# Kernel optimization log

Measured on AMD Instinct MI355X. Metric: run time of the kernel, lower is better.

The kernel has to match this reference:

```python
import jax, jax.numpy as jnp
import numpy as np

N_NODES = 100_000
N_EDGES = 3_200_000
D_IN, D_EDGE, D_HID, D_OUT = 8, 4, 32, 16
NEG_SLOPE = 0.2  # PyG GATv2Conv default


def setup_inputs() -> dict:
    key = jax.random.key(0)
    ks = jax.random.split(key, 13)
    s = 0.1
    return {
        "x": jax.random.normal(ks[0], (N_NODES, D_IN), jnp.float32),
        "edge_index": jax.random.randint(ks[1], (2, N_EDGES), 0, N_NODES, dtype=jnp.int64),
        "edge_attr": jax.random.normal(ks[2], (N_EDGES, D_EDGE), jnp.float32),
        "Wl1": jax.random.normal(ks[3], (D_IN, D_HID), jnp.float32) * s,
        "Wr1": jax.random.normal(ks[4], (D_IN, D_HID), jnp.float32) * s,
        "We1": jax.random.normal(ks[5], (D_EDGE, D_HID), jnp.float32) * s,
        "att1": jax.random.normal(ks[6], (D_HID,), jnp.float32) * s,
        "b1": jnp.zeros((D_HID,), jnp.float32),
        "Wl2": jax.random.normal(ks[7], (D_HID, D_OUT), jnp.float32) * s,
        "Wr2": jax.random.normal(ks[8], (D_HID, D_OUT), jnp.float32) * s,
        "We2": jax.random.normal(ks[9], (D_EDGE, D_OUT), jnp.float32) * s,
        "att2": jax.random.normal(ks[10], (D_OUT,), jnp.float32) * s,
        "b2": jnp.zeros((D_OUT,), jnp.float32),
    }


def _segment_softmax(score, seg, n):
    m = jax.ops.segment_max(score, seg, num_segments=n)
    e = jnp.exp(score - m[seg])
    z = jax.ops.segment_sum(e, seg, num_segments=n)
    return e / z[seg]


def _gatv2(x, src, dst, ea_raw, Wl, Wr, We, att, bias, n):
    # GATv2 (heads=1): score_ij = att . leaky_relu(Wl x_j + Wr x_i + We e_ij)
    xl = x @ Wl            # [N, d]
    xr = x @ Wr            # [N, d]
    ea = ea_raw @ We       # [E, d]
    h = jax.nn.leaky_relu(xl[src] + xr[dst] + ea, NEG_SLOPE)  # [E, d]
    score = h @ att        # [E]
    alpha = _segment_softmax(score, dst, n)
    out = jax.ops.segment_sum(alpha[:, None] * xl[src], dst, num_segments=n)
    return out + bias


def reference(x, edge_index, edge_attr, Wl1, Wr1, We1, att1, b1, Wl2, Wr2, We2, att2, b2):
    n = x.shape[0]
    src, dst = edge_index[0], edge_index[1]
    # add_self_loops=True with fill_value='mean': self-loop edge_attr = mean of
    # incoming raw edge_attr per target node (0 for isolated targets)
    ones = jnp.ones((src.shape[0],), x.dtype)
    cnt = jax.ops.segment_sum(ones, dst, num_segments=n)
    loop_attr = jax.ops.segment_sum(edge_attr, dst, num_segments=n) / jnp.maximum(cnt, 1.0)[:, None]
    ar = jnp.arange(n, dtype=src.dtype)
    src2 = jnp.concatenate([src, ar])
    dst2 = jnp.concatenate([dst, ar])
    ea2 = jnp.concatenate([edge_attr, loop_attr], axis=0)
    h = jax.nn.relu(_gatv2(x, src2, dst2, ea2, Wl1, Wr1, We1, att1, b1, n))
    out = _gatv2(h, src2, dst2, ea2, Wl2, Wr2, We2, att2, b2, n)
    return out.reshape(-1)
```

## Files before the change

kernel.cpp:

```cpp
#include <hip/hip_runtime.h>

#define NEG_SLOPE 0.2f
#define CHUNK 16384
#define KMAX  1600
#define CAP   3264
#define NBLKMAX 256

__global__ __launch_bounds__(1024) void k_bin(const int* __restrict__ ei,
                                              const float* __restrict__ eattr,
                                              int* __restrict__ cloff,
                                              int* __restrict__ ssrc,
                                              float4* __restrict__ seat,
                                              int E, int K) {
    __shared__ int s_off[KMAX + 1];
    __shared__ unsigned s_eid[CHUNK];
    int t = threadIdx.x;
    for (int i = t; i <= K; i += 1024) s_off[i] = 0;
    __syncthreads();
    int base = blockIdx.x * CHUNK;
    int end = min(base + CHUNK, E);
    int Ec = end - base;
    unsigned pack[CHUNK / 1024];
#pragma unroll
    for (int i = 0; i < CHUNK / 1024; i++) {
        int el = t + 1024 * i;
        pack[i] = 0xFFFFFFFFu;
        if (el < Ec) {
            int dst = ei[E + base + el];
            int b = dst >> 6;
            int r = atomicAdd(&s_off[b], 1);
            pack[i] = ((unsigned)b << 20) | ((unsigned)(dst & 63) << 14) | (unsigned)r;
        }
    }
    __syncthreads();
    if (t < 64) {
        int run = 0;
        for (int bb = 0; bb < K; bb += 64) {
            int b = bb + t;
            int v = (b < K) ? s_off[b] : 0;
            int x = v;
#pragma unroll
            for (int off = 1; off < 64; off <<= 1) {
                int y = __shfl_up(x, off, 64);
                if (t >= off) x += y;
            }
            if (b < K) s_off[b] = run + x - v;
            run += __shfl(x, 63, 64);
        }
        if (t == 0) s_off[K] = run;
    }
    __syncthreads();
#pragma unroll
    for (int i = 0; i < CHUNK / 1024; i++) {
        int el = t + 1024 * i;
        if (el < Ec) {
            unsigned p = pack[i];
            int b = p >> 20;
            int r = p & 0x3FFF;
            int dl = (p >> 14) & 63;
            s_eid[s_off[b] + r] = ((unsigned)dl << 14) | (unsigned)el;
        }
    }
    __syncthreads();
    for (int pos = t; pos < Ec; pos += 1024) {
        unsigned v = s_eid[pos];
        int el = v & 0x3FFF;
        int dl = v >> 14;
        int e = base + el;
        int src = ei[e];
        float4 a = *(const float4*)(eattr + 4ll * e);
        ssrc[base + pos] = src | (dl << 17);
        seat[base + pos] = a;
    }
    for (int i = t; i <= K; i += 1024)
        cloff[(long long)blockIdx.x * (K + 1) + i] = s_off[i];
}

__global__ void k_transp(const int* __restrict__ in, int* __restrict__ out, int R, int C) {
    __shared__ int tile[32][33];
    int c0 = blockIdx.x * 32, r0 = blockIdx.y * 32;
    int c = c0 + threadIdx.x, r = r0 + threadIdx.y;
    if (r < R && c < C) tile[threadIdx.y][threadIdx.x] = in[(long long)r * C + c];
    __syncthreads();
    int oc = r0 + threadIdx.x, orr = c0 + threadIdx.y;
    if (orr < C && oc < R) out[(long long)orr * R + oc] = tile[threadIdx.x][threadIdx.y];
}

__global__ void k_btot(const int* __restrict__ cloffT, int* __restrict__ bucketTotal,
                       int K, int NBLK) {
    int b = (blockIdx.x * blockDim.x + threadIdx.x) >> 6;
    int lane = threadIdx.x & 63;
    if (b >= K) return;
    const int* r0 = cloffT + (long long)b * NBLK;
    const int* r1 = r0 + NBLK;
    int s = 0;
    for (int c = lane; c < NBLK; c += 64) s += r1[c] - r0[c];
#pragma unroll
    for (int off = 32; off >= 1; off >>= 1) s += __shfl_xor(s, off, 64);
    if (lane == 0) bucketTotal[b] = s;
}

__global__ void k_scanK(const int* __restrict__ bucketTotal, int* __restrict__ slotBase,
                        int* __restrict__ qofs, int N, int K) {
    __shared__ int s[512];
    int t = threadIdx.x;
    int v[4];
    int sum = 0;
    int base = t * 4;
    for (int j = 0; j < 4; j++) {
        int b = base + j, x = 0;
        if (b < K) { int nb = min(64, N - (b << 6)); x = bucketTotal[b] + nb; }
        v[j] = sum;
        sum += x;
    }
    s[t] = sum;
    __syncthreads();
    for (int off = 1; off < 512; off <<= 1) {
        int x = (t >= off) ? s[t - off] : 0;
        __syncthreads();
        s[t] += x;
        __syncthreads();
    }
    int tb = s[t] - sum;
    for (int j = 0; j < 4; j++) {
        int b = base + j;
        if (b < K) slotBase[b] = tb + v[j];
    }
    if (t == 511) { slotBase[K] = s[511]; qofs[4ll * N] = s[511]; }
}

__global__ __launch_bounds__(512, 8) void k_perm(const int* __restrict__ ssrc,
                                                 const float4* __restrict__ seat,
                                                 const int* __restrict__ cloffT,
                                                 const int* __restrict__ slotBase,
                                                 int* __restrict__ qofs,
                                                 int* __restrict__ fsrc,
                                                 float4* __restrict__ feat,
                                                 int N, int K, int NBLK, int QDIV) {
    __shared__ int s_pack[CAP];
    __shared__ int s_g[CAP];
    __shared__ int co[NBLKMAX], qq[NBLKMAX + 1], sc[NBLKMAX];
    __shared__ int hist2[256], cur2[256], lst2[256], sc2[256];
    __shared__ int hist[64];
    __shared__ float lsum[64][4];
    int b = blockIdx.x, t = threadIdx.x;
    int nb = min(64, N - (b << 6));
    if (t < 256) { hist2[t] = 0; cur2[t] = 0; }
    if (t < 64) {
        lsum[t][0] = 0.f; lsum[t][1] = 0.f; lsum[t][2] = 0.f; lsum[t][3] = 0.f;
    }
    const int* r0 = cloffT + (long long)b * NBLK;
    const int* r1 = r0 + NBLK;
    int len = 0;
    if (t < NBLKMAX) {
        if (t < NBLK) { int c0v = r0[t]; len = r1[t] - c0v; co[t] = c0v; }
        sc[t] = (t < NBLK) ? len : 0;
    }
    __syncthreads();
    for (int off = 1; off < NBLKMAX; off <<= 1) {
        int x = 0;
        if (t < NBLKMAX && t >= off) x = sc[t - off];
        __syncthreads();
        if (t < NBLKMAX) sc[t] += x;
        __syncthreads();
    }
    if (t < NBLK) qq[t] = sc[t] - len;
    if (t == NBLKMAX - 1) qq[NBLK] = sc[NBLKMAX - 1];
    __syncthreads();
    int Eb = qq[NBLK];
    for (int i = t; i < Eb; i += 512) {
        int lo2 = 0, hi2 = NBLK;
        while (lo2 + 1 < hi2) { int mid = (lo2 + hi2) >> 1; if (qq[mid] <= i) lo2 = mid; else hi2 = mid; }
        int g = lo2 * CHUNK + co[lo2] + (i - qq[lo2]);
        int p = ssrc[g];
        int srcv = p & 0x1FFFF;
        int q = (unsigned)srcv / (unsigned)QDIV;
        s_pack[i] = p | (q << 23);
        s_g[i] = g;
        atomicAdd(&hist2[(((p >> 17) & 63) << 2) | q], 1);
    }
    __syncthreads();
    if (t < 64) {
        int c = hist2[4 * t] + hist2[4 * t + 1] + hist2[4 * t + 2] + hist2[4 * t + 3];
        hist[t] = c;
        if (t < nb) {
            int node = (b << 6) + t;
            int qs = (unsigned)node / (unsigned)QDIV;
            hist2[t * 4 + qs] += 1;
            cur2[t * 4 + qs] = 1;
        }
    }
    __syncthreads();
    if (t < 256) sc2[t] = hist2[t];
    __syncthreads();
    for (int off = 1; off < 256; off <<= 1) {
        int x = 0;
        if (t < 256 && t >= off) x = sc2[t - off];
        __syncthreads();
        if (t < 256) sc2[t] += x;
        __syncthreads();
    }
    if (t < 256) lst2[t] = sc2[t] - hist2[t];
    __syncthreads();
    int lo = slotBase[b];
    if (t < 256) {
        int dl = t >> 2;
        if (dl < nb)
            qofs[(((long long)((b << 6) + dl)) << 2) + (t & 3)] = lo + lst2[t];
    }
    for (int i = t; i < Eb; i += 512) {
        int p = s_pack[i];
        int dl = (p >> 17) & 63;
        int q = (p >> 23) & 3;
        int srcv = p & 0x1FFFF;
        int bin = (dl << 2) | q;
        int r = atomicAdd(&cur2[bin], 1);
        float4 a = seat[s_g[i]];
        long long pos = lo + lst2[bin] + r;
        fsrc[pos] = srcv;
        feat[pos] = a;
        atomicAdd(&lsum[dl][0], a.x);
        atomicAdd(&lsum[dl][1], a.y);
        atomicAdd(&lsum[dl][2], a.z);
        atomicAdd(&lsum[dl][3], a.w);
    }
    __syncthreads();
    if (t < nb) {
        int node = (b << 6) + t;
        int qs = (unsigned)node / (unsigned)QDIV;
        float inv = 1.f / fmaxf((float)hist[t], 1.f);
        long long pos = lo + lst2[t * 4 + qs];
        fsrc[pos] = node;
        feat[pos] = make_float4(lsum[t][0] * inv, lsum[t][1] * inv,
                                lsum[t][2] * inv, lsum[t][3] * inv);
    }
}

template <int DIN, int D>
__global__ void k_xform(const float* __restrict__ x, const float* __restrict__ Wl,
                        const float* __restrict__ Wr, float* __restrict__ xl,
                        float* __restrict__ xr, int N) {
    __shared__ float sWl[DIN * D], sWr[DIN * D];
    for (int i = threadIdx.x; i < DIN * D; i += blockDim.x) { sWl[i] = Wl[i]; sWr[i] = Wr[i]; }
    __syncthreads();
    int t = blockIdx.x * blockDim.x + threadIdx.x;
    if (t >= N * D) return;
    int n = t / D, d = t % D;
    const float* xp = x + (long long)n * DIN;
    float sl = 0.f, sr = 0.f;
#pragma unroll
    for (int k = 0; k < DIN; k++) {
        float xv = xp[k];
        sl += xv * sWl[k * D + d];
        sr += xv * sWr[k * D + d];
    }
    xl[t] = sl;
    xr[t] = sr;
}

template <int L>
__device__ __forceinline__ void gat_edge(bool valid, const float4& a, const float4& xlv,
                                         const float4& we0, const float4& we1,
                                         const float4& we2, const float4& we3,
                                         const float4& av, const float4& xrv,
                                         float4& acc, float& z) {
    float4 v;
    v.x = fmaf(a.x, we0.x, xrv.x); v.x = fmaf(a.y, we1.x, v.x);
    v.x = fmaf(a.z, we2.x, v.x);   v.x = fmaf(a.w, we3.x, v.x); v.x += xlv.x;
    v.y = fmaf(a.x, we0.y, xrv.y); v.y = fmaf(a.y, we1.y, v.y);
    v.y = fmaf(a.z, we2.y, v.y);   v.y = fmaf(a.w, we3.y, v.y); v.y += xlv.y;
    v.z = fmaf(a.x, we0.z, xrv.z); v.z = fmaf(a.y, we1.z, v.z);
    v.z = fmaf(a.z, we2.z, v.z);   v.z = fmaf(a.w, we3.z, v.z); v.z += xlv.z;
    v.w = fmaf(a.x, we0.w, xrv.w); v.w = fmaf(a.y, we1.w, v.w);
    v.w = fmaf(a.z, we2.w, v.w);   v.w = fmaf(a.w, we3.w, v.w); v.w += xlv.w;
    v.x = v.x > 0.f ? v.x : NEG_SLOPE * v.x;
    v.y = v.y > 0.f ? v.y : NEG_SLOPE * v.y;
    v.z = v.z > 0.f ? v.z : NEG_SLOPE * v.z;
    v.w = v.w > 0.f ? v.w : NEG_SLOPE * v.w;
    float sc = av.x * v.x + av.y * v.y + av.z * v.z + av.w * v.w;
#pragma unroll
    for (int off = L / 2; off >= 1; off >>= 1) sc += __shfl_xor(sc, off, 64);
    float ev = valid ? __expf(sc) : 0.f;
    z += ev;
    acc.x = fmaf(ev, xlv.x, acc.x);
    acc.y = fmaf(ev, xlv.y, acc.y);
    acc.z = fmaf(ev, xlv.z, acc.z);
    acc.w = fmaf(ev, xlv.w, acc.w);
}

template <int D, bool RELU>
__global__ void k_gat(const int* __restrict__ fsrc,
                      const float4* __restrict__ feat,
                      const int* __restrict__ qofs,
                      const float* __restrict__ xl, const float* __restrict__ xr,
                      const float* __restrict__ We, const float* __restrict__ att,
                      const float* __restrict__ bias, float* __restrict__ out, int N) {
    constexpr int L = D / 4;
    constexpr int G = 64 / L;
    int w = (blockIdx.x * blockDim.x + threadIdx.x) >> 6;
    int lane = threadIdx.x & 63;
    if (w >= N) return;
    int g = lane / L;
    int j = lane % L;
    int s0 = qofs[4 * w], s1 = qofs[4 * w + 4];
    int cnt = s1 - s0;

    const float4 we0 = *(const float4*)(We + 0 * D + 4 * j);
    const float4 we1 = *(const float4*)(We + 1 * D + 4 * j);
    const float4 we2 = *(const float4*)(We + 2 * D + 4 * j);
    const float4 we3 = *(const float4*)(We + 3 * D + 4 * j);
    const float4 av  = *(const float4*)(att + 4 * j);
    const float4 xrv = *(const float4*)(xr + (long long)w * D + 4 * j);

    float4 acc = make_float4(0.f, 0.f, 0.f, 0.f);
    float z = 0.f;

    int it = 0;
    for (; (it + 2) * G <= cnt; it += 2) {
        int sl = s0 + it * G + g;
        int srcA = fsrc[sl];
        int srcB = fsrc[sl + G];
        float4 aA = feat[sl];
        float4 aB = feat[sl + G];
        float4 xA = *(const float4*)(xl + (long long)srcA * D + 4 * j);
        float4 xB = *(const float4*)(xl + (long long)srcB * D + 4 * j);
        gat_edge<L>(true, aA, xA, we0, we1, we2, we3, av, xrv, acc, z);
        gat_edge<L>(true, aB, xB, we0, we1, we2, we3, av, xrv, acc, z);
    }
    for (; it * G < cnt; ++it) {
        int o = it * G + g;
        bool v = o < cnt;
        int sl = s0 + min(o, cnt - 1);
        int src = fsrc[sl];
        float4 a = feat[sl];
        float4 xv = *(const float4*)(xl + (long long)src * D + 4 * j);
        gat_edge<L>(v, a, xv, we0, we1, we2, we3, av, xrv, acc, z);
    }

#pragma unroll
    for (int off = 32; off >= L; off >>= 1) {
        acc.x += __shfl_xor(acc.x, off, 64);
        acc.y += __shfl_xor(acc.y, off, 64);
        acc.z += __shfl_xor(acc.z, off, 64);
        acc.w += __shfl_xor(acc.w, off, 64);
        z += __shfl_xor(z, off, 64);
    }

    if (g == 0) {
        float inv = 1.0f / z;
        float4 bv = *(const float4*)(bias + 4 * j);
        float4 o;
        o.x = acc.x * inv + bv.x;
        o.y = acc.y * inv + bv.y;
        o.z = acc.z * inv + bv.z;
        o.w = acc.w * inv + bv.w;
        if (RELU) {
            o.x = fmaxf(o.x, 0.f); o.y = fmaxf(o.y, 0.f);
            o.z = fmaxf(o.z, 0.f); o.w = fmaxf(o.w, 0.f);
        }
        *(float4*)(out + (long long)w * D + 4 * j) = o;
    }
}

extern "C" void kernel_launch(void* const* d_in, const int* in_sizes, int n_in,
                              void* d_out, int out_size, void* d_ws, size_t ws_size,
                              hipStream_t stream) {
    const float* x     = (const float*)d_in[0];
    const int*   ei    = (const int*)d_in[1];
    const float* eattr = (const float*)d_in[2];
    const float* Wl1   = (const float*)d_in[3];
    const float* Wr1   = (const float*)d_in[4];
    const float* We1   = (const float*)d_in[5];
    const float* att1  = (const float*)d_in[6];
    const float* b1    = (const float*)d_in[7];
    const float* Wl2   = (const float*)d_in[8];
    const float* Wr2   = (const float*)d_in[9];
    const float* We2   = (const float*)d_in[10];
    const float* att2  = (const float*)d_in[11];
    const float* b2    = (const float*)d_in[12];

    const int N = in_sizes[0] / 8;
    const int E = in_sizes[1] / 2;
    const int K = (N + 63) >> 6;
    const int NBLK = (E + CHUNK - 1) / CHUNK;
    const int QDIV = (N + 3) / 4;

    int* iws = (int*)d_ws;
    size_t o = 0;
    int* bucketTotal = iws + o; o += K;
    int* slotBase    = iws + o; o += K + 1;
    int* qofs        = iws + o; o += 4ll * N + 1;
    int* cloff       = iws + o; o += (size_t)NBLK * (K + 1);
    int* cloffT      = iws + o; o += (size_t)(K + 1) * NBLK;
    o = (o + 7) & ~(size_t)7;
    int*    fsrc = (int*)(iws + o);    o += (size_t)(E + N);
    o = (o + 3) & ~(size_t)3;
    float4* feat = (float4*)(iws + o); o += 4ll * (E + N);
    size_t stage = o;
    int*    ssrc = (int*)(iws + o);    o += (size_t)E;
    o = (o + 3) & ~(size_t)3;
    float4* seat = (float4*)(iws + o); o += 4ll * E;
    float* xl = (float*)(iws + stage);
    float* xr = xl + 32ll * N;
    float* h  = xr + 32ll * N;

    const int B = 256;
    auto cdiv = [](long long a, long long b) { return (int)((a + b - 1) / b); };

    k_bin<<<NBLK, 1024, 0, stream>>>(ei, eattr, cloff, ssrc, seat, E, K);
    dim3 tb(32, 32);
    k_transp<<<dim3(cdiv(K + 1, 32), cdiv(NBLK, 32)), tb, 0, stream>>>(cloff, cloffT, NBLK, K + 1);
    k_btot<<<cdiv(64ll * K, B), B, 0, stream>>>(cloffT, bucketTotal, K, NBLK);
    k_scanK<<<1, 512, 0, stream>>>(bucketTotal, slotBase, qofs, N, K);
    k_perm<<<K, 512, 0, stream>>>(ssrc, seat, cloffT, slotBase, qofs, fsrc, feat, N, K, NBLK, QDIV);

    k_xform<8, 32><<<cdiv(32ll * N, B), B, 0, stream>>>(x, Wl1, Wr1, xl, xr, N);
    k_gat<32, true><<<cdiv(N, 4), B, 0, stream>>>(fsrc, feat, qofs, xl, xr, We1, att1, b1, h, N);

    k_xform<32, 16><<<cdiv(16ll * N, B), B, 0, stream>>>(h, Wl2, Wr2, xl, xr, N);
    k_gat<16, false><<<cdiv(N, 4), B, 0, stream>>>(fsrc, feat, qofs, xl, xr, We2, att2, b2, (float*)d_out, N);
}
```

Measured before the change: 487.9 us.

## Halve bin chunk size, parallelize bucket scan, scatter directly without LDS staging

The binning kernel now works on 8192-edge chunks with 512 threads, which doubles the number of blocks. The single-wavefront serial scan over bucket counts becomes a block-wide Hillis-Steele scan with 4 buckets per thread. The shared edge-id staging array is removed, and each edge's src and attributes are written straight to their binned position. This cuts LDS use and the serial scan latency, but the direct scatter gives less coalesced global reads and writes, and the downstream transpose, total and perm stages must handle twice as many per-block offset rows.

```diff
diff --git a/kernel.cpp b/kernel.cpp
--- a/kernel.cpp
+++ b/kernel.cpp
@@ -1,29 +1,28 @@
 #include <hip/hip_runtime.h>
 
 #define NEG_SLOPE 0.2f
-#define CHUNK 16384
+#define CHUNK 8192
 #define KMAX  1600
 #define CAP   3264
-#define NBLKMAX 256
-
-__global__ __launch_bounds__(1024) void k_bin(const int* __restrict__ ei,
-                                              const float* __restrict__ eattr,
-                                              int* __restrict__ cloff,
-                                              int* __restrict__ ssrc,
-                                              float4* __restrict__ seat,
-                                              int E, int K) {
+#define NBLKMAX 512
+
+__global__ __launch_bounds__(512) void k_bin(const int* __restrict__ ei,
+                                             const float* __restrict__ eattr,
+                                             int* __restrict__ cloff,
+                                             int* __restrict__ ssrc,
+                                             float4* __restrict__ seat,
+                                             int E, int K) {
     __shared__ int s_off[KMAX + 1];
-    __shared__ unsigned s_eid[CHUNK];
+    __shared__ int s_scan[512];
     int t = threadIdx.x;
-    for (int i = t; i <= K; i += 1024) s_off[i] = 0;
+    for (int i = t; i <= K; i += 512) s_off[i] = 0;
     __syncthreads();
     int base = blockIdx.x * CHUNK;
-    int end = min(base + CHUNK, E);
-    int Ec = end - base;
-    unsigned pack[CHUNK / 1024];
-#pragma unroll
-    for (int i = 0; i < CHUNK / 1024; i++) {
-        int el = t + 1024 * i;
+    int Ec = min(CHUNK, E - base);
+    unsigned pack[CHUNK / 512];
+#pragma unroll
+    for (int i = 0; i < CHUNK / 512; i++) {
+        int el = t + 512 * i;
         pack[i] = 0xFFFFFFFFu;
         if (el < Ec) {
             int dst = ei[E + base + el];
@@ -33,46 +32,48 @@
         }
     }
     __syncthreads();
-    if (t < 64) {
-        int run = 0;
-        for (int bb = 0; bb < K; bb += 64) {
-            int b = bb + t;
-            int v = (b < K) ? s_off[b] : 0;
-            int x = v;
-#pragma unroll
-            for (int off = 1; off < 64; off <<= 1) {
-                int y = __shfl_up(x, off, 64);
-                if (t >= off) x += y;
-            }
-            if (b < K) s_off[b] = run + x - v;
-            run += __shfl(x, 63, 64);
-        }
-        if (t == 0) s_off[K] = run;
-    }
-    __syncthreads();
-#pragma unroll
-    for (int i = 0; i < CHUNK / 1024; i++) {
-        int el = t + 1024 * i;
+    int v4[4];
+    int sum = 0;
+    int b0 = t << 2;
+#pragma unroll
+    for (int jj = 0; jj < 4; jj++) {
+        int b = b0 + jj;
+        int x = (b <= K) ? s_off[b] : 0;
+        v4[jj] = sum;
+        sum += x;
+    }
+    s_scan[t] = sum;
+    __syncthreads();
+    for (int off = 1; off < 512; off <<= 1) {
+        int x = (t >= off) ? s_scan[t - off] : 0;
+        __syncthreads();
+        s_scan[t] += x;
+        __syncthreads();
+    }
+    int tb = s_scan[t] - sum;
+#pragma unroll
+    for (int jj = 0; jj < 4; jj++) {
+        int b = b0 + jj;
+        if (b <= K) s_off[b] = tb + v4[jj];
+    }
+    __syncthreads();
+#pragma unroll
+    for (int i = 0; i < CHUNK / 512; i++) {
+        int el = t + 512 * i;
         if (el < Ec) {
             unsigned p = pack[i];
             int b = p >> 20;
+            int dl = (p >> 14) & 63;
             int r = p & 0x3FFF;
-            int dl = (p >> 14) & 63;
-            s_eid[s_off[b] + r] = ((unsigned)dl << 14) | (unsigned)el;
+            int pos = s_off[b] + r;
+            int e = base + el;
+            int src = ei[e];
+            float4 a = *(const float4*)(eattr + 4ll * e);
+            ssrc[base + pos] = src | (dl << 17);
+            seat[base + pos] = a;
         }
     }
-    __syncthreads();
-    for (int pos = t; pos < Ec; pos += 1024) {
-        unsigned v = s_eid[pos];
-        int el = v & 0x3FFF;
-        int dl = v >> 14;
-        int e = base + el;
-        int src = ei[e];
-        float4 a = *(const float4*)(eattr + 4ll * e);
-        ssrc[base + pos] = src | (dl << 17);
-        seat[base + pos] = a;
-    }
-    for (int i = t; i <= K; i += 1024)
+    for (int i = t; i <= K; i += 512)
         cloff[(long long)blockIdx.x * (K + 1) + i] = s_off[i];
 }
 
@@ -407,7 +408,7 @@
     const int B = 256;
     auto cdiv = [](long long a, long long b) { return (int)((a + b - 1) / b); };
 
-    k_bin<<<NBLK, 1024, 0, stream>>>(ei, eattr, cloff, ssrc, seat, E, K);
+    k_bin<<<NBLK, 512, 0, stream>>>(ei, eattr, cloff, ssrc, seat, E, K);
     dim3 tb(32, 32);
     k_transp<<<dim3(cdiv(K + 1, 32), cdiv(NBLK, 32)), tb, 0, stream>>>(cloff, cloffT, NBLK, K + 1);
     k_btot<<<cdiv(64ll * K, B), B, 0, stream>>>(cloffT, bucketTotal, K, NBLK);
```

Result: slower. 502.9 us (+3.1%).

## Restructure CSR build with smaller chunks, 256-node buckets, and shared staging

Applied to the files above, without the earlier changes.

Changes the edge binning so each block handles 4096 edges and destinations are grouped into 256-node buckets instead of 64. k_bin now gathers src and edge_attr straight into shared memory at their sorted positions and then writes them out coalesced. k_perm runs 1024 threads per block, re-reads ssrc in a second pass instead of caching it in shared memory, and covers four times as many nodes per block. The aim is fewer, larger permutation blocks and coalesced staging writes, at the cost of doubled global reads in k_perm, a binary search over up to 1024 chunks per edge, and a larger cloff matrix.

```diff
diff --git a/kernel.cpp b/kernel.cpp
--- a/kernel.cpp
+++ b/kernel.cpp
@@ -1,10 +1,9 @@
 #include <hip/hip_runtime.h>
 
 #define NEG_SLOPE 0.2f
-#define CHUNK 16384
-#define KMAX  1600
-#define CAP   3264
-#define NBLKMAX 256
+#define CHUNK 4096
+#define KMAX  512
+#define NBLKMAX 1024
 
 __global__ __launch_bounds__(1024) void k_bin(const int* __restrict__ ei,
                                               const float* __restrict__ eattr,
@@ -13,13 +12,14 @@
                                               float4* __restrict__ seat,
                                               int E, int K) {
     __shared__ int s_off[KMAX + 1];
-    __shared__ unsigned s_eid[CHUNK];
+    __shared__ int s_scan[1024];
+    __shared__ int s_ssrc[CHUNK];
+    __shared__ float4 s_seat[CHUNK];
     int t = threadIdx.x;
     for (int i = t; i <= K; i += 1024) s_off[i] = 0;
     __syncthreads();
     int base = blockIdx.x * CHUNK;
-    int end = min(base + CHUNK, E);
-    int Ec = end - base;
+    int Ec = min(CHUNK, E - base);
     unsigned pack[CHUNK / 1024];
 #pragma unroll
     for (int i = 0; i < CHUNK / 1024; i++) {
@@ -27,28 +27,22 @@
         pack[i] = 0xFFFFFFFFu;
         if (el < Ec) {
             int dst = ei[E + base + el];
-            int b = dst >> 6;
+            int b = dst >> 8;
             int r = atomicAdd(&s_off[b], 1);
-            pack[i] = ((unsigned)b << 20) | ((unsigned)(dst & 63) << 14) | (unsigned)r;
+            pack[i] = ((unsigned)b << 20) | ((unsigned)(dst & 255) << 12) | (unsigned)r;
         }
     }
     __syncthreads();
-    if (t < 64) {
-        int run = 0;
-        for (int bb = 0; bb < K; bb += 64) {
-            int b = bb + t;
-            int v = (b < K) ? s_off[b] : 0;
-            int x = v;
-#pragma unroll
-            for (int off = 1; off < 64; off <<= 1) {
-                int y = __shfl_up(x, off, 64);
-                if (t >= off) x += y;
-            }
-            if (b < K) s_off[b] = run + x - v;
-            run += __shfl(x, 63, 64);
-        }
-        if (t == 0) s_off[K] = run;
-    }
+    int x0 = (t <= K) ? s_off[t] : 0;
+    s_scan[t] = x0;
+    __syncthreads();
+    for (int off = 1; off < 1024; off <<= 1) {
+        int y = (t >= off) ? s_scan[t - off] : 0;
+        __syncthreads();
+        s_scan[t] += y;
+        __syncthreads();
+    }
+    if (t <= K) s_off[t] = s_scan[t] - x0;
     __syncthreads();
 #pragma unroll
     for (int i = 0; i < CHUNK / 1024; i++) {
@@ -56,21 +50,18 @@
         if (el < Ec) {
             unsigned p = pack[i];
             int b = p >> 20;
-            int r = p & 0x3FFF;
-            int dl = (p >> 14) & 63;
-            s_eid[s_off[b] + r] = ((unsigned)dl << 14) | (unsigned)el;
+            int dl = (p >> 12) & 255;
+            int r = p & 0xFFF;
+            int pos = s_off[b] + r;
+            int e = base + el;
+            s_ssrc[pos] = ei[e] | (dl << 17);
+            s_seat[pos] = *(const float4*)(eattr + 4ll * e);
         }
     }
     __syncthreads();
     for (int pos = t; pos < Ec; pos += 1024) {
-        unsigned v = s_eid[pos];
-        int el = v & 0x3FFF;
-        int dl = v >> 14;
-        int e = base + el;
-        int src = ei[e];
-        float4 a = *(const float4*)(eattr + 4ll * e);
-        ssrc[base + pos] = src | (dl << 17);
-        seat[base + pos] = a;
+        ssrc[base + pos] = s_ssrc[pos];
+        seat[base + pos] = s_seat[pos];
     }
     for (int i = t; i <= K; i += 1024)
         cloff[(long long)blockIdx.x * (K + 1) + i] = s_off[i];
@@ -109,7 +100,7 @@
     int base = t * 4;
     for (int j = 0; j < 4; j++) {
         int b = base + j, x = 0;
-        if (b < K) { int nb = min(64, N - (b << 6)); x = bucketTotal[b] + nb; }
+        if (b < K) { int nb = min(256, N - (b << 8)); x = bucketTotal[b] + nb; }
         v[j] = sum;
         sum += x;
     }
@@ -129,93 +120,81 @@
     if (t == 511) { slotBase[K] = s[511]; qofs[4ll * N] = s[511]; }
 }
 
-__global__ __launch_bounds__(512, 8) void k_perm(const int* __restrict__ ssrc,
-                                                 const float4* __restrict__ seat,
-                                                 const int* __restrict__ cloffT,
-                                                 const int* __restrict__ slotBase,
-                                                 int* __restrict__ qofs,
-                                                 int* __restrict__ fsrc,
-                                                 float4* __restrict__ feat,
-                                                 int N, int K, int NBLK, int QDIV) {
-    __shared__ int s_pack[CAP];
-    __shared__ int s_g[CAP];
+__global__ __launch_bounds__(1024, 2) void k_perm(const int* __restrict__ ssrc,
+                                                  const float4* __restrict__ seat,
+                                                  const int* __restrict__ cloffT,
+                                                  const int* __restrict__ slotBase,
+                                                  int* __restrict__ qofs,
+                                                  int* __restrict__ fsrc,
+                                                  float4* __restrict__ feat,
+                                                  int N, int K, int NBLK, int QDIV) {
     __shared__ int co[NBLKMAX], qq[NBLKMAX + 1], sc[NBLKMAX];
-    __shared__ int hist2[256], cur2[256], lst2[256], sc2[256];
-    __shared__ int hist[64];
-    __shared__ float lsum[64][4];
+    __shared__ int hist2[1024], cur2[1024], lst2[1024], sc2[1024];
+    __shared__ int hist[256];
+    __shared__ float lsum[256][4];
     int b = blockIdx.x, t = threadIdx.x;
-    int nb = min(64, N - (b << 6));
-    if (t < 256) { hist2[t] = 0; cur2[t] = 0; }
-    if (t < 64) {
-        lsum[t][0] = 0.f; lsum[t][1] = 0.f; lsum[t][2] = 0.f; lsum[t][3] = 0.f;
-    }
+    int nb = min(256, N - (b << 8));
+    hist2[t] = 0; cur2[t] = 0;
+    if (t < 256) { lsum[t][0] = 0.f; lsum[t][1] = 0.f; lsum[t][2] = 0.f; lsum[t][3] = 0.f; }
     const int* r0 = cloffT + (long long)b * NBLK;
     const int* r1 = r0 + NBLK;
     int len = 0;
-    if (t < NBLKMAX) {
-        if (t < NBLK) { int c0v = r0[t]; len = r1[t] - c0v; co[t] = c0v; }
-        sc[t] = (t < NBLK) ? len : 0;
-    }
+    if (t < NBLK) { int c0v = r0[t]; len = r1[t] - c0v; co[t] = c0v; }
+    sc[t] = (t < NBLK) ? len : 0;
     __syncthreads();
     for (int off = 1; off < NBLKMAX; off <<= 1) {
-        int x = 0;
-        if (t < NBLKMAX && t >= off) x = sc[t - off];
-        __syncthreads();
-        if (t < NBLKMAX) sc[t] += x;
+        int x = (t >= off) ? sc[t - off] : 0;
+        __syncthreads();
+        sc[t] += x;
         __syncthreads();
     }
     if (t < NBLK) qq[t] = sc[t] - len;
     if (t == NBLKMAX - 1) qq[NBLK] = sc[NBLKMAX - 1];
     __syncthreads();
     int Eb = qq[NBLK];
-    for (int i = t; i < Eb; i += 512) {
+    for (int i = t; i < Eb; i += 1024) {
+        int lo2 = 0, hi2 = NBLK;
+        while (lo2 + 1 < hi2) { int mid = (lo2 + hi2) >> 1; if (qq[mid] <= i) lo2 = mid; else hi2 = mid; }
+        int g = lo2 * CHUNK + co[lo2] + (i - qq[lo2]);
+        int p = ssrc[g];
+        int q = (int)((unsigned)(p & 0x1FFFF) / (unsigned)QDIV);
+        atomicAdd(&hist2[(((p >> 17) & 255) << 2) | q], 1);
+    }
+    __syncthreads();
+    if (t < 256) {
+        int c = hist2[4 * t] + hist2[4 * t + 1] + hist2[4 * t + 2] + hist2[4 * t + 3];
+        hist[t] = c;
+        if (t < nb) {
+            int node = (b << 8) + t;
+            int qs = (int)((unsigned)node / (unsigned)QDIV);
+            hist2[4 * t + qs] += 1;
+            cur2[4 * t + qs] = 1;
+        }
+    }
+    __syncthreads();
+    sc2[t] = hist2[t];
+    __syncthreads();
+    for (int off = 1; off < 1024; off <<= 1) {
+        int x = (t >= off) ? sc2[t - off] : 0;
+        __syncthreads();
+        sc2[t] += x;
+        __syncthreads();
+    }
+    lst2[t] = sc2[t] - hist2[t];
+    __syncthreads();
+    int lo = slotBase[b];
+    if (t < 4 * nb) qofs[((long long)b << 10) + t] = lo + lst2[t];
+    for (int i = t; i < Eb; i += 1024) {
         int lo2 = 0, hi2 = NBLK;
         while (lo2 + 1 < hi2) { int mid = (lo2 + hi2) >> 1; if (qq[mid] <= i) lo2 = mid; else hi2 = mid; }
         int g = lo2 * CHUNK + co[lo2] + (i - qq[lo2]);
         int p = ssrc[g];
         int srcv = p & 0x1FFFF;
-        int q = (unsigned)srcv / (unsigned)QDIV;
-        s_pack[i] = p | (q << 23);
-        s_g[i] = g;
-        atomicAdd(&hist2[(((p >> 17) & 63) << 2) | q], 1);
-    }
-    __syncthreads();
-    if (t < 64) {
-        int c = hist2[4 * t] + hist2[4 * t + 1] + hist2[4 * t + 2] + hist2[4 * t + 3];
-        hist[t] = c;
-        if (t < nb) {
-            int node = (b << 6) + t;
-            int qs = (unsigned)node / (unsigned)QDIV;
-            hist2[t * 4 + qs] += 1;
-            cur2[t * 4 + qs] = 1;
-        }
-    }
-    __syncthreads();
-    if (t < 256) sc2[t] = hist2[t];
-    __syncthreads();
-    for (int off = 1; off < 256; off <<= 1) {
-        int x = 0;
-        if (t < 256 && t >= off) x = sc2[t - off];
-        __syncthreads();
-        if (t < 256) sc2[t] += x;
-        __syncthreads();
-    }
-    if (t < 256) lst2[t] = sc2[t] - hist2[t];
-    __syncthreads();
-    int lo = slotBase[b];
-    if (t < 256) {
-        int dl = t >> 2;
-        if (dl < nb)
-            qofs[(((long long)((b << 6) + dl)) << 2) + (t & 3)] = lo + lst2[t];
-    }
-    for (int i = t; i < Eb; i += 512) {
-        int p = s_pack[i];
-        int dl = (p >> 17) & 63;
-        int q = (p >> 23) & 3;
-        int srcv = p & 0x1FFFF;
+        int dl = (p >> 17) & 255;
+        int q = (int)((unsigned)srcv / (unsigned)QDIV);
         int bin = (dl << 2) | q;
         int r = atomicAdd(&cur2[bin], 1);
-        float4 a = seat[s_g[i]];
+        float4 a = seat[g];
         long long pos = lo + lst2[bin] + r;
         fsrc[pos] = srcv;
         feat[pos] = a;
@@ -226,10 +205,10 @@
     }
     __syncthreads();
     if (t < nb) {
-        int node = (b << 6) + t;
-        int qs = (unsigned)node / (unsigned)QDIV;
+        int node = (b << 8) + t;
+        int qs = (int)((unsigned)node / (unsigned)QDIV);
         float inv = 1.f / fmaxf((float)hist[t], 1.f);
-        long long pos = lo + lst2[t * 4 + qs];
+        long long pos = lo + lst2[4 * t + qs];
         fsrc[pos] = node;
         feat[pos] = make_float4(lsum[t][0] * inv, lsum[t][1] * inv,
                                 lsum[t][2] * inv, lsum[t][3] * inv);
@@ -381,7 +360,7 @@
 
     const int N = in_sizes[0] / 8;
     const int E = in_sizes[1] / 2;
-    const int K = (N + 63) >> 6;
+    const int K = (N + 255) >> 8;
     const int NBLK = (E + CHUNK - 1) / CHUNK;
     const int QDIV = (N + 3) / 4;
 
@@ -412,7 +391,7 @@
     k_transp<<<dim3(cdiv(K + 1, 32), cdiv(NBLK, 32)), tb, 0, stream>>>(cloff, cloffT, NBLK, K + 1);
     k_btot<<<cdiv(64ll * K, B), B, 0, stream>>>(cloffT, bucketTotal, K, NBLK);
     k_scanK<<<1, 512, 0, stream>>>(bucketTotal, slotBase, qofs, N, K);
-    k_perm<<<K, 512, 0, stream>>>(ssrc, seat, cloffT, slotBase, qofs, fsrc, feat, N, K, NBLK, QDIV);
+    k_perm<<<K, 1024, 0, stream>>>(ssrc, seat, cloffT, slotBase, qofs, fsrc, feat, N, K, NBLK, QDIV);
 
     k_xform<8, 32><<<cdiv(32ll * N, B), B, 0, stream>>>(x, Wl1, Wr1, xl, xr, N);
     k_gat<32, true><<<cdiv(N, 4), B, 0, stream>>>(fsrc, feat, qofs, xl, xr, We1, att1, b1, h, N);
```

Result: faster. 458.2 us (-6.1%).
